# Performance work log

Measured on AMD Instinct MI355X. Metric: run time of the kernel, lower is better.

## Reference

```python
import jax, jax.numpy as jnp
import numpy as np

GRID = 0.5
NG = 48
NC = 16  # output channels
CHUNK = 256  # atoms per scan step (bounds peak memory)
E2 = float(np.exp(2.0))
# order matches pro_keys ['O','C','N','S'] with vdw_dic
VDW = jnp.array([1.52, 1.7, 1.55, 1.8], dtype=jnp.float32)


def setup_inputs() -> dict:
    key = jax.random.key(0)
    k1, k2, k3 = jax.random.split(key, 3)
    N = 2048
    coords = jax.random.uniform(k1, (N, 3), dtype=jnp.float32) * (NG * GRID)  # [0, 24)
    ch_idx = jax.random.randint(k2, (N,), 0, 4, dtype=jnp.int32)
    fg = jax.random.randint(k3, (N,), 0, 16, dtype=jnp.int32)
    return {"coords": coords, "ch_idx": ch_idx, "fg": fg}


def _channel_weights(ch_idx, fg):
    # base element channel 0..3
    w = jax.nn.one_hot(ch_idx, NC, dtype=jnp.float32)
    # fg routing: 14 -> +ch4 +ch5; 15 -> +ch6 +ch9; 12/13 -> nothing; else -> +ch(fg+4)
    c1 = jnp.where(fg == 14, 4, jnp.where(fg == 15, 6, fg + 4))
    c1 = jnp.where((fg == 12) | (fg == 13), -1, c1)  # one_hot(-1) == zeros
    c2 = jnp.where(fg == 14, 5, jnp.where(fg == 15, 9, -1))
    return w + jax.nn.one_hot(c1, NC, dtype=jnp.float32) + jax.nn.one_hot(c2, NC, dtype=jnp.float32)


def _grid_forward(coords, r, w):
    # coords [N,3], r [N] vdw radii, w [N,16] channel weights -> [16,48,48,48]
    gx = GRID * jnp.arange(NG, dtype=jnp.float32)  # grid point coordinates
    nchunk = coords.shape[0] // CHUNK
    coords_c = coords.reshape(nchunk, CHUNK, 3)
    r_c = r.reshape(nchunk, CHUNK)
    w_c = w.reshape(nchunk, CHUNK, NC)

    def body(acc, args):
        c, rr, ww = args  # [CHUNK,3], [CHUNK], [CHUNK,16]
        dx2 = (c[:, 0, None] - gx) ** 2  # [CHUNK,48]
        dy2 = (c[:, 1, None] - gx) ** 2
        dz2 = (c[:, 2, None] - gx) ** 2
        d2 = dx2[:, :, None, None] + dy2[:, None, :, None] + dz2[:, None, None, :]  # [CHUNK,48,48,48]
        d = jnp.sqrt(d2)
        r_ = rr[:, None, None, None]
        r2 = r_ * r_
        f1 = jnp.exp(-2.0 * d2 / r2)
        f2 = 4.0 * d2 / (E2 * r2) - 12.0 * d / (E2 * r_) + 9.0 / E2
        val = jnp.where(d < r_, f1, jnp.where(d < 1.5 * r_, f2, 0.0))
        acc = acc + jnp.einsum('nc,nxyz->cxyz', ww, val)
        return acc, None

    out, _ = jax.lax.scan(body, jnp.zeros((NC, NG, NG, NG), jnp.float32), (coords_c, r_c, w_c))
    return out


def reference(coords, ch_idx, fg):
    r = VDW[ch_idx]
    w = _channel_weights(ch_idx, fg)
    return _grid_forward(coords, r, w)
```

## Files before the change

### kernel.cpp

```cpp
#include <hip/hip_runtime.h>

#define NG 48
#define NC 16
#define NPTS (NG * NG * NG)
#define E2F 7.3890561f
#define NINE_OVER_E2 1.2180176f
#define LOG2E 1.44269504f

#define SEGCAP 48

__device__ __forceinline__ float sel_r(int ci) {
    return ci == 0 ? 1.52f : ci == 1 ? 1.7f : ci == 2 ? 1.55f : 1.8f;
}
__device__ __forceinline__ int chan_mask(int ci, int f) {
    int c1 = (f == 14) ? 4 : ((f == 15) ? 6 : f + 4);
    if (f == 12 || f == 13) c1 = -1;
    const int c2 = (f == 14) ? 5 : ((f == 15) ? 9 : -1);
    int mask = 1 << ci;
    if (c1 >= 0) mask |= 1 << c1;
    if (c2 >= 0) mask |= 1 << c2;
    return mask;
}

__global__ __launch_bounds__(256)
void density_fused_kernel(const float* __restrict__ coords,
                          const int* __restrict__ ch_idx,
                          const int* __restrict__ fg,
                          float* __restrict__ out, int natoms)
{
    __shared__ float4 sA[4 * SEGCAP];
    __shared__ float4 sB[4 * SEGCAP];
    __shared__ float sRed[4 * NC][64];

    const int t = threadIdx.x, w = t >> 6, l = t & 63;
    const int bz = blockIdx.x, by = blockIdx.y, bx = blockIdx.z;

    const float lox = bx * 2.0f, hix = lox + 1.5f;
    const float loy = by * 2.0f, hiy = loy + 1.5f;
    const float loz = bz * 2.0f, hiz = loz + 1.5f;

    const int quarter = (natoms + 3) >> 2;
    const int a0 = w * quarter;
    const int a1 = min(a0 + quarter, natoms);
    int cnt = 0;
    #pragma unroll 4
    for (int base = a0; base < a1; base += 64) {
        const int a = base + l;
        bool pred = false;
        float ax = 0.f, ay = 0.f, az = 0.f, r = 1.f, cut = 0.f;
        int ci = 0;
        if (a < a1) {
            ax = coords[3 * a]; ay = coords[3 * a + 1]; az = coords[3 * a + 2];
            ci = ch_idx[a];
            r = sel_r(ci);
            cut = 1.5f * r;
            const float ddx = fmaxf(fmaxf(lox - ax, ax - hix), 0.f);
            const float ddy = fmaxf(fmaxf(loy - ay, ay - hiy), 0.f);
            const float ddz = fmaxf(fmaxf(loz - az, az - hiz), 0.f);
            pred = fmaf(ddx, ddx, fmaf(ddy, ddy, ddz * ddz)) < cut * cut;
        }
        const unsigned long long m = __ballot(pred);
        if (pred) {
            const int o = cnt + __popcll(m & ((1ull << l) - 1ull));
            if (o < SEGCAP) {
                const float r2 = r * r;
                const int f = fg[a];
                sA[w * SEGCAP + o] = make_float4(ax, ay, az, cut);
                sB[w * SEGCAP + o] = make_float4(-2.0f * LOG2E / r2,
                                                 4.0f / (E2F * r2),
                                                 12.0f / (E2F * r),
                                                 __int_as_float(chan_mask(ci, f)));
            }
        }
        cnt += __popcll(m);
    }
    cnt = min(cnt, SEGCAP);

    const int tz = l & 3, ty = (l >> 2) & 3, tx = l >> 4;
    const float px = (bx * 4 + tx) * 0.5f;
    const float py = (by * 4 + ty) * 0.5f;
    const float pz = (bz * 4 + tz) * 0.5f;

    float acc[NC];
    #pragma unroll
    for (int c = 0; c < NC; ++c) acc[c] = 0.0f;

    const int segbase = w * SEGCAP;
    float4 A0, B0;
    if (cnt > 0) { A0 = sA[segbase]; B0 = sB[segbase]; }
    for (int i = 0; i < cnt; ++i) {
        float4 A1 = A0, B1 = B0;
        if (i + 1 < cnt) { A1 = sA[segbase + i + 1]; B1 = sB[segbase + i + 1]; }
        const float dx = px - A0.x;
        const float dy = py - A0.y;
        const float dz = pz - A0.z;
        const float d2 = fmaf(dx, dx, fmaf(dy, dy, dz * dz));
        const float cut2 = A0.w * A0.w;
        const float r2 = cut2 * (4.0f / 9.0f);
        const float d  = sqrtf(d2);
        const float f1 = exp2f(B0.x * d2);
        const float f2 = fmaf(B0.y, d2, fmaf(-B0.z, d, NINE_OVER_E2));
        float val = (d2 < r2) ? f1 : f2;
        val = (d2 < cut2) ? val : 0.0f;
        const int chan = __builtin_amdgcn_readfirstlane(__float_as_int(B0.w));
        #pragma unroll
        for (int c = 0; c < NC; ++c) {
            const float msk = __int_as_float(((chan >> c) & 1) * 0x3f800000);
            acc[c] = fmaf(msk, val, acc[c]);
        }
        A0 = A1; B0 = B1;
    }

    #pragma unroll
    for (int c = 0; c < NC; ++c) sRed[w * NC + c][l] = acc[c];
    __syncthreads();

    const int chl = l >> 4;
    const int xy  = l & 15;
    const int c   = w * 4 + chl;
    float4 s = *(const float4*)&sRed[0 * NC + c][xy * 4];
    const float4 s1 = *(const float4*)&sRed[1 * NC + c][xy * 4];
    const float4 s2 = *(const float4*)&sRed[2 * NC + c][xy * 4];
    const float4 s3 = *(const float4*)&sRed[3 * NC + c][xy * 4];
    s.x += s1.x + s2.x + s3.x;
    s.y += s1.y + s2.y + s3.y;
    s.z += s1.z + s2.z + s3.z;
    s.w += s1.w + s2.w + s3.w;

    const int gx = bx * 4 + (xy >> 2);
    const int gy = by * 4 + (xy & 3);
    const int gz0 = bz * 4;
    *(float4*)&out[c * NPTS + (gx * NG + gy) * NG + gz0] = s;
}

extern "C" void kernel_launch(void* const* d_in, const int* in_sizes, int n_in,
                              void* d_out, int out_size, void* d_ws, size_t ws_size,
                              hipStream_t stream) {
    (void)n_in; (void)out_size; (void)d_ws; (void)ws_size;
    const float* coords = (const float*)d_in[0];
    const int* ch = (const int*)d_in[1];
    const int* fgp = (const int*)d_in[2];
    float* out = (float*)d_out;
    const int natoms = in_sizes[0] / 3;

    dim3 grid(NG / 4, NG / 4, NG / 4);
    density_fused_kernel<<<grid, 256, 0, stream>>>(coords, ch, fgp, out, natoms);
}
```

Before: 24.25 us.

## Split atom binning into separate build kernel writing per-brick lists to workspace

Measured after the change: 27.10 us. +11.8%, slower.

```diff
diff --git a/kernel.cpp b/kernel.cpp
--- a/kernel.cpp
+++ b/kernel.cpp
@@ -7,6 +7,7 @@
 #define NINE_OVER_E2 1.2180176f
 #define LOG2E 1.44269504f
 
+#define SUBCAP 32
 #define SEGCAP 48
 
 __device__ __forceinline__ float sel_r(int ci) {
@@ -20,6 +21,134 @@
     if (c1 >= 0) mask |= 1 << c1;
     if (c2 >= 0) mask |= 1 << c2;
     return mask;
+}
+
+__global__ __launch_bounds__(256)
+void build_kernel(const float* __restrict__ coords,
+                  const int* __restrict__ ch_idx,
+                  const int* __restrict__ fg,
+                  float4* __restrict__ segAB,
+                  int* __restrict__ counts, int natoms)
+{
+    const int t = threadIdx.x, w = t >> 6, l = t & 63;
+    const int b = blockIdx.x;
+    const int bx = b / 144, by = (b / 12) % 12, bz = b % 12;
+
+    const float lox = bx * 2.0f, hix = lox + 1.5f;
+    const float loy = by * 2.0f, hiy = loy + 1.5f;
+    const float loz = bz * 2.0f, hiz = loz + 1.5f;
+
+    const int quarter = (natoms + 3) >> 2;
+    const int a0 = w * quarter;
+    const int a1 = min(a0 + quarter, natoms);
+    const int segbase = (b * 4 + w) * SUBCAP;
+
+    int cnt = 0;
+    #pragma unroll 4
+    for (int base = a0; base < a1; base += 64) {
+        const int a = base + l;
+        bool pred = false;
+        float ax = 0.f, ay = 0.f, az = 0.f, r = 1.f, cut = 0.f;
+        int ci = 0;
+        if (a < a1) {
+            ax = coords[3 * a]; ay = coords[3 * a + 1]; az = coords[3 * a + 2];
+            ci = ch_idx[a];
+            r = sel_r(ci);
+            cut = 1.5f * r;
+            const float ddx = fmaxf(fmaxf(lox - ax, ax - hix), 0.f);
+            const float ddy = fmaxf(fmaxf(loy - ay, ay - hiy), 0.f);
+            const float ddz = fmaxf(fmaxf(loz - az, az - hiz), 0.f);
+            pred = fmaf(ddx, ddx, fmaf(ddy, ddy, ddz * ddz)) < cut * cut;
+        }
+        const unsigned long long m = __ballot(pred);
+        if (pred) {
+            const int o = cnt + __popcll(m & ((1ull << l) - 1ull));
+            if (o < SUBCAP) {
+                const float r2 = r * r;
+                const int f = fg[a];
+                segAB[(segbase + o) * 2 + 0] = make_float4(ax, ay, az, cut);
+                segAB[(segbase + o) * 2 + 1] = make_float4(-2.0f * LOG2E / r2,
+                                                           4.0f / (E2F * r2),
+                                                           12.0f / (E2F * r),
+                                                           __int_as_float(chan_mask(ci, f)));
+            }
+        }
+        cnt += __popcll(m);
+    }
+    if (l == 0) counts[b * 4 + w] = min(cnt, SUBCAP);
+}
+
+__global__ __launch_bounds__(256, 8)
+void density_kernel(const float4* __restrict__ segAB,
+                    const int* __restrict__ counts,
+                    float* __restrict__ out)
+{
+    __shared__ float sRed[4 * NC][64];
+
+    const int t = threadIdx.x, w = t >> 6, l = t & 63;
+    const int bz = blockIdx.x, by = blockIdx.y, bx = blockIdx.z;
+    const int b = (bx * 12 + by) * 12 + bz;
+
+    const int cw = counts[b * 4 + w];
+    const int segbase = (b * 4 + w) * SUBCAP;
+
+    const int tz = l & 3, ty = (l >> 2) & 3, tx = l >> 4;
+    const float px = (bx * 4 + tx) * 0.5f;
+    const float py = (by * 4 + ty) * 0.5f;
+    const float pz = (bz * 4 + tz) * 0.5f;
+
+    float acc[NC];
+    #pragma unroll
+    for (int c = 0; c < NC; ++c) acc[c] = 0.0f;
+
+    float4 A0, B0;
+    if (cw > 0) { A0 = segAB[segbase * 2]; B0 = segAB[segbase * 2 + 1]; }
+    for (int i = 0; i < cw; ++i) {
+        float4 A1 = A0, B1 = B0;
+        if (i + 1 < cw) {
+            A1 = segAB[(segbase + i + 1) * 2];
+            B1 = segAB[(segbase + i + 1) * 2 + 1];
+        }
+        const float dx = px - A0.x;
+        const float dy = py - A0.y;
+        const float dz = pz - A0.z;
+        const float d2 = fmaf(dx, dx, fmaf(dy, dy, dz * dz));
+        const float cut2 = A0.w * A0.w;
+        const float r2 = cut2 * (4.0f / 9.0f);
+        const float d  = sqrtf(d2);
+        const float f1 = exp2f(B0.x * d2);
+        const float f2 = fmaf(B0.y, d2, fmaf(-B0.z, d, NINE_OVER_E2));
+        float val = (d2 < r2) ? f1 : f2;
+        val = (d2 < cut2) ? val : 0.0f;
+        const int chan = __builtin_amdgcn_readfirstlane(__float_as_int(B0.w));
+        #pragma unroll
+        for (int c = 0; c < NC; ++c) {
+            const float msk = __int_as_float(((chan >> c) & 1) * 0x3f800000);
+            acc[c] = fmaf(msk, val, acc[c]);
+        }
+        A0 = A1; B0 = B1;
+    }
+
+    #pragma unroll
+    for (int c = 0; c < NC; ++c) sRed[w * NC + c][l] = acc[c];
+    __syncthreads();
+
+    const int chl = l >> 4;
+    const int xy  = l & 15;
+    const int c   = w * 4 + chl;
+    float4 s = *(const float4*)&sRed[0 * NC + c][xy * 4];
+    const float4 s1 = *(const float4*)&sRed[1 * NC + c][xy * 4];
+    const float4 s2 = *(const float4*)&sRed[2 * NC + c][xy * 4];
+    const float4 s3 = *(const float4*)&sRed[3 * NC + c][xy * 4];
+    s.x += s1.x + s2.x + s3.x;
+    s.y += s1.y + s2.y + s3.y;
+    s.z += s1.z + s2.z + s3.z;
+    s.w += s1.w + s2.w + s3.w;
+
+    const int gx = bx * 4 + (xy >> 2);
+    const int gy = by * 4 + (xy & 3);
+    const int gz0 = bz * 4;
+    *(float4*)&out[c * NPTS + (gx * NG + gy) * NG + gz0] = s;
 }
 
 __global__ __launch_bounds__(256)
@@ -136,13 +265,24 @@
 extern "C" void kernel_launch(void* const* d_in, const int* in_sizes, int n_in,
                               void* d_out, int out_size, void* d_ws, size_t ws_size,
                               hipStream_t stream) {
-    (void)n_in; (void)out_size; (void)d_ws; (void)ws_size;
+    (void)n_in; (void)out_size;
     const float* coords = (const float*)d_in[0];
     const int* ch = (const int*)d_in[1];
     const int* fgp = (const int*)d_in[2];
     float* out = (float*)d_out;
     const int natoms = in_sizes[0] / 3;
 
-    dim3 grid(NG / 4, NG / 4, NG / 4);
-    density_fused_kernel<<<grid, 256, 0, stream>>>(coords, ch, fgp, out, natoms);
-}
+    const int nbricks = 12 * 12 * 12;
+    const size_t cnt_bytes = ((size_t)nbricks * 4 * sizeof(int) + 255) & ~255ull;
+    const size_t need = cnt_bytes + (size_t)nbricks * 4 * SUBCAP * 2 * sizeof(float4);
+    dim3 grid(12, 12, 12);
+
+    if (ws_size >= need) {
+        int* counts = (int*)d_ws;
+        float4* segAB = (float4*)((char*)d_ws + cnt_bytes);
+        build_kernel<<<nbricks, 256, 0, stream>>>(coords, ch, fgp, segAB, counts, natoms);
+        density_kernel<<<grid, 256, 0, stream>>>(segAB, counts, out);
+    } else {
+        density_fused_kernel<<<grid, 256, 0, stream>>>(coords, ch, fgp, out, natoms);
+    }
+}
```
